# Kernel optimization log

Measured on AMD Instinct MI355X. Metric: run time of the kernel, lower is better.

The kernel has to match this reference:

```python
import jax, jax.numpy as jnp
import numpy as np

N, E, G = 50000, 200000, 1000
EPS = 1e-5
NEG_SLOPE = 0.2


def setup_inputs() -> dict:
    key = jax.random.key(0)
    ks = jax.random.split(key, 24)
    p = lambda k, shape: jax.random.normal(k, shape, jnp.float32) * 0.05
    inp = {
        "x": jax.random.normal(ks[0], (N, 64), jnp.float32),
        "edge_index": jax.random.randint(ks[1], (2, E), 0, N, jnp.int32),
        "batch": jnp.sort(jax.random.randint(ks[2], (N,), 0, G, jnp.int32)),
        "solvent_fingerprint": jax.random.uniform(ks[3], (G, 128), jnp.float32),
        # GAT layer 1: 64 -> 4 heads x 128
        "W1": p(ks[4], (64, 512)), "a1_src": p(ks[5], (4, 128)), "a1_dst": p(ks[6], (4, 128)), "b1": jnp.zeros((512,), jnp.float32),
        "bn1_g": jnp.ones((512,), jnp.float32), "bn1_b": jnp.zeros((512,), jnp.float32),
        # GAT layer 2: 512 -> 4 heads x 256
        "W2": p(ks[7], (512, 1024)), "a2_src": p(ks[8], (4, 256)), "a2_dst": p(ks[9], (4, 256)), "b2": jnp.zeros((1024,), jnp.float32),
        "bn2_g": jnp.ones((1024,), jnp.float32), "bn2_b": jnp.zeros((1024,), jnp.float32),
        # GCN: 1024 -> 256
        "Wg": p(ks[10], (1024, 256)), "bg": jnp.zeros((256,), jnp.float32),
        "bn3_g": jnp.ones((256,), jnp.float32), "bn3_b": jnp.zeros((256,), jnp.float32),
        # MLP head
        "Ws": p(ks[11], (128, 128)), "bs": jnp.zeros((128,), jnp.float32),
        "Wf1": p(ks[12], (640, 128)), "bf1": jnp.zeros((128,), jnp.float32),
        "bnf_g": jnp.ones((128,), jnp.float32), "bnf_b": jnp.zeros((128,), jnp.float32),
        "Wf2": p(ks[13], (128, 1)), "bf2": jnp.zeros((1,), jnp.float32),
    }
    return inp


def _batchnorm(x, g, b):
    mu = x.mean(0)
    var = x.var(0)
    return (x - mu) * jax.lax.rsqrt(var + EPS) * g + b


def _gat(x, src, dst, W, a_src, a_dst, b, H, C):
    n = x.shape[0]
    h = (x @ W).reshape(n, H, C)                      # [N,H,C]
    al_s = (h * a_src).sum(-1)                        # [N,H]
    al_d = (h * a_dst).sum(-1)                        # [N,H]
    e = jax.nn.leaky_relu(al_s[src] + al_d[dst], NEG_SLOPE)   # [E,H]
    m = jax.ops.segment_max(e, dst, num_segments=n)
    ex = jnp.exp(e - m[dst])
    s = jax.ops.segment_sum(ex, dst, num_segments=n)
    alpha = ex / jnp.maximum(s[dst], 1e-16)
    out = jax.ops.segment_sum(h[src] * alpha[..., None], dst, num_segments=n)  # [N,H,C]
    return out.reshape(n, H * C) + b


def _gcn(x, src, dst, W, b):
    n = x.shape[0]
    h = x @ W
    deg = jax.ops.segment_sum(jnp.ones_like(dst, jnp.float32), dst, num_segments=n)
    dinv = jax.lax.rsqrt(jnp.maximum(deg, 1.0))
    norm = dinv[src] * dinv[dst]
    return jax.ops.segment_sum(h[src] * norm[:, None], dst, num_segments=n) + b


def reference(x, edge_index, batch, solvent_fingerprint,
              W1, a1_src, a1_dst, b1, bn1_g, bn1_b,
              W2, a2_src, a2_dst, b2, bn2_g, bn2_b,
              Wg, bg, bn3_g, bn3_b,
              Ws, bs, Wf1, bf1, bnf_g, bnf_b, Wf2, bf2):
    n = x.shape[0]
    loops = jnp.arange(n, dtype=edge_index.dtype)
    src = jnp.concatenate([edge_index[0], loops])
    dst = jnp.concatenate([edge_index[1], loops])

    h = _gat(x, src, dst, W1, a1_src, a1_dst, b1, 4, 128)
    h = jax.nn.relu(_batchnorm(h, bn1_g, bn1_b))
    h = _gat(h, src, dst, W2, a2_src, a2_dst, b2, 4, 256)
    h = jax.nn.relu(_batchnorm(h, bn2_g, bn2_b))
    h = _gcn(h, src, dst, Wg, bg)
    h = jax.nn.relu(_batchnorm(h, bn3_g, bn3_b))

    cnt = jax.ops.segment_sum(jnp.ones((n,), jnp.float32), batch, num_segments=G)
    gap = jax.ops.segment_sum(h, batch, num_segments=G) / jnp.maximum(cnt, 1.0)[:, None]
    gmp = jax.ops.segment_max(h, batch, num_segments=G)
    gmp = jnp.where(jnp.isfinite(gmp), gmp, 0.0)

    solv = jax.nn.relu(solvent_fingerprint @ Ws + bs)
    z = jnp.concatenate([gap, gmp, solv], axis=1)          # [G,640]
    z = jax.nn.relu(_batchnorm(z @ Wf1 + bf1, bnf_g, bnf_b))
    # dropout: identity in eval/deterministic reference
    return jax.nn.sigmoid(z @ Wf2 + bf2)
```

## Files before the change

kernel.cpp:

```cpp
#include <hip/hip_runtime.h>
#include <cmath>

#define LEAK 0.2f
#define BN_EPS 1e-5f

static inline int cdiv(long long a, long long b){ return (int)((a + b - 1) / b); }

typedef __attribute__((ext_vector_type(8))) short bf16x8;
typedef __attribute__((ext_vector_type(4))) float f32x4;

__device__ __forceinline__ float bf2f(unsigned short u){
    return __uint_as_float(((unsigned int)u) << 16);
}
__device__ __forceinline__ unsigned short f2bf(float f){
    unsigned int u = __float_as_uint(f);
    u += 0x7FFFu + ((u >> 16) & 1u);
    return (unsigned short)(u >> 16);
}

#define GLOAD_LDS16(gsrc, ldst) \
    __builtin_amdgcn_global_load_lds( \
        (const __attribute__((address_space(1))) unsigned int*)(gsrc), \
        (__attribute__((address_space(3))) unsigned int*)(ldst), 16, 0, 0)

__global__ __launch_bounds__(256) void gemm_mfma(
    const unsigned short* __restrict__ A, const unsigned short* __restrict__ Bt,
    unsigned short* __restrict__ D, int M, int K, int lda, int ldb, int ldc,
    int NX, int NYT)
{
    const int id = blockIdx.x;
    const int xcd = id & 7;
    const int j = id >> 3;
    const int bx = j % NX;
    const int by = (j / NX) * 8 + xcd;
    if (by >= NYT) return;

    __shared__ unsigned short As[128 * 64];
    __shared__ unsigned short Bs[128 * 64];
    const int t = threadIdx.x;
    const int row0 = by * 128, col0 = bx * 128;
    const int lane = t & 63, wv = t >> 6;
    const int wm = (wv >> 1) << 6, wn = (wv & 1) << 6;
    const int lm = lane & 15, lq = lane >> 4;

    const int sr  = t >> 3;
    const int scs = (t & 7) << 3;
    const int gsw = (((t & 7) ^ (sr & 7)) << 3);
    const unsigned short* ap[4];
    const unsigned short* bp[4];
    unsigned short* la[4];
    unsigned short* lb[4];
    #pragma unroll
    for (int q = 0; q < 4; ++q) {
        int r = sr + q * 32;
        int gra = row0 + r; if (gra >= M) gra = M - 1;
        ap[q] = A  + (size_t)gra * lda + gsw;
        bp[q] = Bt + (size_t)(col0 + r) * ldb + gsw;
        la[q] = &As[r * 64 + scs];
        lb[q] = &Bs[r * 64 + scs];
    }

    f32x4 acc[4][4] = {};
    const int rx = lm & 7;

    for (int k0 = 0; k0 < K; k0 += 64) {
        #pragma unroll
        for (int q = 0; q < 4; ++q) {
            GLOAD_LDS16(ap[q] + k0, la[q]);
            GLOAD_LDS16(bp[q] + k0, lb[q]);
        }
        __syncthreads();

        #pragma unroll
        for (int kk = 0; kk < 2; ++kk) {
            const int ck = (((kk << 2) + lq) ^ rx) << 3;
            bf16x8 af[4], bfr[4];
            #pragma unroll
            for (int mi = 0; mi < 4; ++mi)
                af[mi] = *(const bf16x8*)&As[(wm + mi * 16 + lm) * 64 + ck];
            #pragma unroll
            for (int ni = 0; ni < 4; ++ni)
                bfr[ni] = *(const bf16x8*)&Bs[(wn + ni * 16 + lm) * 64 + ck];
            #pragma unroll
            for (int mi = 0; mi < 4; ++mi)
                #pragma unroll
                for (int ni = 0; ni < 4; ++ni)
                    acc[mi][ni] = __builtin_amdgcn_mfma_f32_16x16x32_bf16(
                        af[mi], bfr[ni], acc[mi][ni], 0, 0, 0);
        }
        __syncthreads();
    }

    #pragma unroll
    for (int mi = 0; mi < 4; ++mi) {
        int row_b = row0 + wm + mi * 16 + lq * 4;
        #pragma unroll
        for (int ni = 0; ni < 4; ++ni) {
            int col = col0 + wn + ni * 16 + lm;
            #pragma unroll
            for (int r = 0; r < 4; ++r) {
                int row = row_b + r;
                if (row < M) D[(size_t)row * ldc + col] = f2bf(acc[mi][ni][r]);
            }
        }
    }
}

__global__ __launch_bounds__(256) void logits_valu(
    const unsigned short* __restrict__ A, const unsigned short* __restrict__ vat,
    float* __restrict__ C, int M, int K)
{
    __shared__ unsigned short vs[8 * 512];
    const int t = threadIdx.x;
    for (int i = t; i < K; i += 256)
        *(bf16x8*)&vs[i * 8] = *(const bf16x8*)(vat + (size_t)i * 8);
    __syncthreads();

    const int lane = t & 63;
    const int w = blockIdx.x * 4 + (t >> 6);
    const int Gl = K >> 3;
    const int rpw = 64 / Gl;
    const int sub = lane / Gl;
    const int li = lane - sub * Gl;
    long long row = (long long)w * rpw + sub;
    if (row >= M) return;

    bf16x8 hv = *(const bf16x8*)(A + row * K + li * 8);
    float hf[8];
    #pragma unroll
    for (int j = 0; j < 8; ++j) hf[j] = bf2f((unsigned short)hv[j]);

    float s[8];
    #pragma unroll
    for (int o = 0; o < 8; ++o) {
        bf16x8 v = *(const bf16x8*)&vs[o * K + li * 8];
        float acc = 0.f;
        #pragma unroll
        for (int j = 0; j < 8; ++j) acc += hf[j] * bf2f((unsigned short)v[j]);
        s[o] = acc;
    }
    for (int off = Gl >> 1; off; off >>= 1) {
        #pragma unroll
        for (int o = 0; o < 8; ++o) s[o] += __shfl_xor(s[o], off);
    }
    #pragma unroll
    for (int o = 0; o < 8; ++o)
        if (li == o) C[row * 8 + o] = s[o];
}

__global__ void convT(const float* __restrict__ W, unsigned short* __restrict__ Wt, int K, int Nc)
{
    int i = blockIdx.x * blockDim.x + threadIdx.x;
    if (i >= K * Nc) return;
    int k = i / Nc, n = i - k * Nc;
    Wt[(size_t)n * K + k] = f2bf(W[i]);
}

template<bool RELU>
__global__ __launch_bounds__(256) void gemm_small(
    const float* __restrict__ A, const float* __restrict__ B,
    const float* __restrict__ bias, float* __restrict__ C,
    int M, int K, int lda, int ldb, int ldc)
{
    __shared__ float As[2][640];
    const int t = threadIdx.x;
    const int r = t >> 7, c = t & 127;
    const int row0 = blockIdx.x * 2;
    for (int i = t; i < 2 * K; i += 256) {
        int rr = i / K, kk = i - rr * K;
        int gr = row0 + rr;
        As[rr][kk] = (gr < M) ? A[(size_t)gr * lda + kk] : 0.f;
    }
    __syncthreads();
    float acc0 = 0.f, acc1 = 0.f;
    for (int k = 0; k < K; k += 8) {
        float4 a0 = *reinterpret_cast<const float4*>(&As[r][k]);
        float4 a1 = *reinterpret_cast<const float4*>(&As[r][k + 4]);
        acc0 += a0.x * B[(size_t)(k + 0) * ldb + c];
        acc1 += a0.y * B[(size_t)(k + 1) * ldb + c];
        acc0 += a0.z * B[(size_t)(k + 2) * ldb + c];
        acc1 += a0.w * B[(size_t)(k + 3) * ldb + c];
        acc0 += a1.x * B[(size_t)(k + 4) * ldb + c];
        acc1 += a1.y * B[(size_t)(k + 5) * ldb + c];
        acc0 += a1.z * B[(size_t)(k + 6) * ldb + c];
        acc1 += a1.w * B[(size_t)(k + 7) * ldb + c];
    }
    int row = row0 + r;
    if (row < M) {
        float v = acc0 + acc1;
        if (bias) v += bias[c];
        if (RELU) v = fmaxf(v, 0.f);
        C[(size_t)row * ldc + c] = v;
    }
}

__global__ void compute_va_bf(const float* __restrict__ W, const float* __restrict__ a_s,
                              const float* __restrict__ a_d, unsigned short* __restrict__ vat,
                              int K, int HC, int C)
{
    int w = (int)(((long long)blockIdx.x * blockDim.x + threadIdx.x) >> 6);
    int lane = threadIdx.x & 63;
    if (w >= K * 4) return;
    int k = w >> 2, h = w & 3;
    const float* wp = W + (size_t)k * HC + h * C;
    const float* as = a_s + h * C;
    const float* ad = a_d + h * C;
    float s = 0.f, d = 0.f;
    for (int c = lane; c < C; c += 64) {
        float v = wp[c];
        s += v * as[c];
        d += v * ad[c];
    }
    #pragma unroll
    for (int off = 32; off; off >>= 1) {
        s += __shfl_down(s, off);
        d += __shfl_down(d, off);
    }
    if (lane == 0) {
        vat[(size_t)h * K + k] = f2bf(s);
        vat[(size_t)(4 + h) * K + k] = f2bf(d);
    }
}

__device__ __forceinline__ int e_src(const int* es, int E, int k){ return k < E ? es[k] : k - E; }
__device__ __forceinline__ int e_dst(const int* ed, int E, int k){ return k < E ? ed[k] : k - E; }

__global__ void fill_i32(int* __restrict__ p, int v, int n)
{
    int i = blockIdx.x * blockDim.x + threadIdx.x;
    if (i < n) p[i] = v;
}

__global__ void hist_dst(const int* __restrict__ ed, int E, int* __restrict__ cnt)
{
    int k = blockIdx.x * blockDim.x + threadIdx.x;
    if (k < E) atomicAdd(&cnt[ed[k]], 1);
}

__global__ __launch_bounds__(256) void scan_blk(const int* __restrict__ cnt,
                                                int* __restrict__ rowptr,
                                                int* __restrict__ bsums, int n)
{
    __shared__ int ts[256];
    const int t = threadIdx.x;
    const int i0 = blockIdx.x * 1024 + t * 4;
    int4 v = {0, 0, 0, 0};
    if (i0 + 3 < n) v = *reinterpret_cast<const int4*>(cnt + i0);
    else {
        if (i0 + 0 < n) v.x = cnt[i0 + 0];
        if (i0 + 1 < n) v.y = cnt[i0 + 1];
        if (i0 + 2 < n) v.z = cnt[i0 + 2];
        if (i0 + 3 < n) v.w = cnt[i0 + 3];
    }
    int lsum = v.x + v.y + v.z + v.w;
    ts[t] = lsum;
    __syncthreads();
    #pragma unroll
    for (int off = 1; off < 256; off <<= 1) {
        int u = (t >= off) ? ts[t - off] : 0;
        __syncthreads();
        ts[t] += u;
        __syncthreads();
    }
    int excl = ts[t] - lsum;
    if (i0 + 0 < n) rowptr[i0 + 0] = excl;
    if (i0 + 1 < n) rowptr[i0 + 1] = excl + v.x;
    if (i0 + 2 < n) rowptr[i0 + 2] = excl + v.x + v.y;
    if (i0 + 3 < n) rowptr[i0 + 3] = excl + v.x + v.y + v.z;
    if (t == 255) bsums[blockIdx.x] = ts[255];
}

__global__ __launch_bounds__(256) void scan_tops(int* __restrict__ bsums,
                                                 int* __restrict__ rowptr, int nb, int n)
{
    __shared__ int ts[256];
    const int t = threadIdx.x;
    int v = (t < nb) ? bsums[t] : 0;
    ts[t] = v;
    __syncthreads();
    #pragma unroll
    for (int off = 1; off < 256; off <<= 1) {
        int u = (t >= off) ? ts[t - off] : 0;
        __syncthreads();
        ts[t] += u;
        __syncthreads();
    }
    if (t < nb) bsums[t] = ts[t] - v;
    if (t == 255) rowptr[n] = ts[255];
}

__global__ void scan_add(int* __restrict__ rowptr, int* __restrict__ cursor,
                         const int* __restrict__ bsums, int n)
{
    int i = blockIdx.x * blockDim.x + threadIdx.x;
    if (i >= n) return;
    int r = rowptr[i] + bsums[i >> 10];
    rowptr[i] = r;
    cursor[i] = r;
}

__global__ void csr_scatter(const int* __restrict__ es, const int* __restrict__ ed,
                            int E, int Etot, int* __restrict__ cursor,
                            int* __restrict__ col, int* __restrict__ dstarr)
{
    int k = blockIdx.x * blockDim.x + threadIdx.x;
    if (k >= Etot) return;
    int sn = e_src(es, E, k), dn = e_dst(ed, E, k);
    int pos = atomicAdd(&cursor[dn], 1);
    col[pos] = sn;
    dstarr[pos] = dn;
}

__global__ void dinv_from_rowptr(const int* __restrict__ rowptr, float* __restrict__ dinv, int n)
{
    int i = blockIdx.x * blockDim.x + threadIdx.x;
    if (i < n) dinv[i] = rsqrtf(fmaxf((float)(rowptr[i + 1] - rowptr[i]), 1.f));
}

__global__ void grp_lb(const int* __restrict__ batch, int N, int G_, int* __restrict__ gptr)
{
    int g = blockIdx.x * blockDim.x + threadIdx.x;
    if (g > G_) return;
    if (g == G_) { gptr[G_] = N; return; }
    int lo = 0, hi = N;
    while (lo < hi) { int mid = (lo + hi) >> 1; if (batch[mid] < g) lo = mid + 1; else hi = mid; }
    gptr[g] = lo;
}

__global__ void edge_exp4(const int* __restrict__ col, const int* __restrict__ dstarr,
                          int Etot, const float* __restrict__ alsd, float* __restrict__ exq)
{
    int p = blockIdx.x * blockDim.x + threadIdx.x;
    if (p >= Etot) return;
    int sn = col[p], dn = dstarr[p];
    #pragma unroll
    for (int h = 0; h < 4; ++h) {
        float t = alsd[sn * 8 + h] + alsd[dn * 8 + 4 + h];
        t = (t >= 0.f) ? t : LEAK * t;
        exq[(size_t)h * Etot + p] = __expf(t);
    }
}

__global__ void gat_gather_all(const int* __restrict__ rowptr, const int* __restrict__ col,
                               const unsigned short* __restrict__ h,
                               const float* __restrict__ exq, int Etot,
                               unsigned short* __restrict__ out, int N)
{
    int w = (int)(((long long)blockIdx.x * blockDim.x + threadIdx.x) >> 6);
    int lane = threadIdx.x & 63;
    if (w >= N) return;
    const float* exp_p = exq + (size_t)(lane >> 4) * Etot;
    int r0 = rowptr[w], r1 = rowptr[w + 1];
    float acc[8] = {};
    float ssum = 0.f;
    int e = r0;
    for (; e + 1 < r1; e += 2) {
        int sn0 = col[e], sn1 = col[e + 1];
        float a0 = exp_p[e], a1 = exp_p[e + 1];
        bf16x8 hv0 = *(const bf16x8*)(h + (size_t)sn0 * 512 + lane * 8);
        bf16x8 hv1 = *(const bf16x8*)(h + (size_t)sn1 * 512 + lane * 8);
        ssum += a0 + a1;
        #pragma unroll
        for (int j = 0; j < 8; ++j)
            acc[j] += bf2f((unsigned short)hv0[j]) * a0 + bf2f((unsigned short)hv1[j]) * a1;
    }
    if (e < r1) {
        int sn = col[e];
        float a = exp_p[e];
        bf16x8 hv = *(const bf16x8*)(h + (size_t)sn * 512 + lane * 8);
        ssum += a;
        #pragma unroll
        for (int j = 0; j < 8; ++j) acc[j] += bf2f((unsigned short)hv[j]) * a;
    }
    float inv = 1.f / fmaxf(ssum, 1e-16f);
    bf16x8 o;
    #pragma unroll
    for (int j = 0; j < 8; ++j) o[j] = (short)f2bf(acc[j] * inv);
    *(bf16x8*)(out + (size_t)w * 512 + lane * 8) = o;
}

__global__ void gat_gather512_bf2(const int* __restrict__ rowptr, const int* __restrict__ col,
                                  const unsigned short* __restrict__ h, int ldh,
                                  const float* __restrict__ exq0, const float* __restrict__ exq1,
                                  unsigned short* __restrict__ out, int N)
{
    int w = (int)(((long long)blockIdx.x * blockDim.x + threadIdx.x) >> 6);
    int lane = threadIdx.x & 63;
    if (w >= N) return;
    int r0 = rowptr[w], r1 = rowptr[w + 1];
    float s0 = 0.f, s1 = 0.f;
    float a00=0.f,a01=0.f,a02=0.f,a03=0.f;
    float a10=0.f,a11=0.f,a12=0.f,a13=0.f;
    int e = r0;
    for (; e + 1 < r1; e += 2) {
        int sA = col[e], sB = col[e + 1];
        float w0A = exq0[e], w0B = exq0[e + 1];
        float w1A = exq1[e], w1B = exq1[e + 1];
        const unsigned short* pA = h + (size_t)sA * ldh + lane * 4;
        const unsigned short* pB = h + (size_t)sB * ldh + lane * 4;
        ushort4 hA0 = *reinterpret_cast<const ushort4*>(pA);
        ushort4 hA1 = *reinterpret_cast<const ushort4*>(pA + 256);
        ushort4 hB0 = *reinterpret_cast<const ushort4*>(pB);
        ushort4 hB1 = *reinterpret_cast<const ushort4*>(pB + 256);
        s0 += w0A + w0B; s1 += w1A + w1B;
        a00 += bf2f(hA0.x) * w0A + bf2f(hB0.x) * w0B;
        a01 += bf2f(hA0.y) * w0A + bf2f(hB0.y) * w0B;
        a02 += bf2f(hA0.z) * w0A + bf2f(hB0.z) * w0B;
        a03 += bf2f(hA0.w) * w0A + bf2f(hB0.w) * w0B;
        a10 += bf2f(hA1.x) * w1A + bf2f(hB1.x) * w1B;
        a11 += bf2f(hA1.y) * w1A + bf2f(hB1.y) * w1B;
        a12 += bf2f(hA1.z) * w1A + bf2f(hB1.z) * w1B;
        a13 += bf2f(hA1.w) * w1A + bf2f(hB1.w) * w1B;
    }
    if (e < r1) {
        int sA = col[e];
        float w0A = exq0[e], w1A = exq1[e];
        const unsigned short* pA = h + (size_t)sA * ldh + lane * 4;
        ushort4 hA0 = *reinterpret_cast<const ushort4*>(pA);
        ushort4 hA1 = *reinterpret_cast<const ushort4*>(pA + 256);
        s0 += w0A; s1 += w1A;
        a00 += bf2f(hA0.x) * w0A; a01 += bf2f(hA0.y) * w0A;
        a02 += bf2f(hA0.z) * w0A; a03 += bf2f(hA0.w) * w0A;
        a10 += bf2f(hA1.x) * w1A; a11 += bf2f(hA1.y) * w1A;
        a12 += bf2f(hA1.z) * w1A; a13 += bf2f(hA1.w) * w1A;
    }
    float i0 = 1.f / fmaxf(s0, 1e-16f);
    float i1 = 1.f / fmaxf(s1, 1e-16f);
    ushort4 o0, o1;
    o0.x = f2bf(a00 * i0); o0.y = f2bf(a01 * i0);
    o0.z = f2bf(a02 * i0); o0.w = f2bf(a03 * i0);
    o1.x = f2bf(a10 * i1); o1.y = f2bf(a11 * i1);
    o1.z = f2bf(a12 * i1); o1.w = f2bf(a13 * i1);
    unsigned short* op = out + (size_t)w * 512 + lane * 4;
    *reinterpret_cast<ushort4*>(op)       = o0;
    *reinterpret_cast<ushort4*>(op + 256) = o1;
}

__global__ void gcn_gather256(const int* __restrict__ rowptr, const int* __restrict__ col,
                              const unsigned short* __restrict__ h,
                              const float* __restrict__ dinv,
                              unsigned short* __restrict__ out, int N)
{
    int w = (int)(((long long)blockIdx.x * blockDim.x + threadIdx.x) >> 6);
    int lane = threadIdx.x & 63;
    if (w >= N) return;
    int r0 = rowptr[w], r1 = rowptr[w + 1];
    float a0 = 0.f, a1 = 0.f, a2 = 0.f, a3 = 0.f;
    int e = r0;
    for (; e + 1 < r1; e += 2) {
        int sn0 = col[e], sn1 = col[e + 1];
        float w0 = dinv[sn0], w1 = dinv[sn1];
        ushort4 hv0 = *reinterpret_cast<const ushort4*>(h + (size_t)sn0 * 256 + lane * 4);
        ushort4 hv1 = *reinterpret_cast<const ushort4*>(h + (size_t)sn1 * 256 + lane * 4);
        a0 += bf2f(hv0.x) * w0 + bf2f(hv1.x) * w1;
        a1 += bf2f(hv0.y) * w0 + bf2f(hv1.y) * w1;
        a2 += bf2f(hv0.z) * w0 + bf2f(hv1.z) * w1;
        a3 += bf2f(hv0.w) * w0 + bf2f(hv1.w) * w1;
    }
    if (e < r1) {
        int sn = col[e];
        float wv = dinv[sn];
        ushort4 hv = *reinterpret_cast<const ushort4*>(h + (size_t)sn * 256 + lane * 4);
        a0 += bf2f(hv.x) * wv; a1 += bf2f(hv.y) * wv;
        a2 += bf2f(hv.z) * wv; a3 += bf2f(hv.w) * wv;
    }
    float dn = dinv[w];
    ushort4 o;
    o.x = f2bf(a0 * dn); o.y = f2bf(a1 * dn);
    o.z = f2bf(a2 * dn); o.w = f2bf(a3 * dn);
    *reinterpret_cast<ushort4*>(out + (size_t)w * 256 + lane * 4) = o;
}

template<int D>
__global__ __launch_bounds__(256) void bn_part(
    const float* __restrict__ x, float* __restrict__ ps, float* __restrict__ pq,
    int M, int Y)
{
    constexpr int DG = D / 4;
    constexpr int P  = 256 / DG;
    const int t = threadIdx.x;
    const int cg = t % DG, ph = t / DG;
    const int y = blockIdx.y;
    const int rows_per = (M + Y - 1) / Y;
    const int r0 = y * rows_per;
    const int r1 = min(r0 + rows_per, M);
    float s0=0,s1=0,s2=0,s3=0,q0=0,q1=0,q2=0,q3=0;
    for (int r = r0 + ph; r < r1; r += P) {
        float4 v = *reinterpret_cast<const float4*>(x + (size_t)r * D + cg * 4);
        s0+=v.x; s1+=v.y; s2+=v.z; s3+=v.w;
        q0+=v.x*v.x; q1+=v.y*v.y; q2+=v.z*v.z; q3+=v.w*v.w;
    }
    __shared__ float ls[P][D];
    __shared__ float lq[P][D];
    ls[ph][cg*4+0]=s0; ls[ph][cg*4+1]=s1; ls[ph][cg*4+2]=s2; ls[ph][cg*4+3]=s3;
    lq[ph][cg*4+0]=q0; lq[ph][cg*4+1]=q1; lq[ph][cg*4+2]=q2; lq[ph][cg*4+3]=q3;
    __syncthreads();
    if (ph == 0) {
        #pragma unroll
        for (int j = 0; j < 4; ++j) {
            float ss = 0.f, qq = 0.f;
            #pragma unroll
            for (int p = 0; p < P; ++p) { ss += ls[p][cg*4+j]; qq += lq[p][cg*4+j]; }
            ps[(size_t)y * D + cg*4 + j] = ss;
            pq[(size_t)y * D + cg*4 + j] = qq;
        }
    }
}

template<int D>
__global__ __launch_bounds__(256) void bn_part_bf(
    const unsigned short* __restrict__ x, int ldx,
    float* __restrict__ ps, float* __restrict__ pq, int M, int Y)
{
    constexpr int DG = D / 4;
    constexpr int P  = 256 / DG;
    const int t = threadIdx.x;
    const int cg = t % DG, ph = t / DG;
    const int y = blockIdx.y;
    const int rows_per = (M + Y - 1) / Y;
    const int r0 = y * rows_per;
    const int r1 = min(r0 + rows_per, M);
    float s0=0,s1=0,s2=0,s3=0,q0=0,q1=0,q2=0,q3=0;
    for (int r = r0 + ph; r < r1; r += P) {
        ushort4 u = *reinterpret_cast<const ushort4*>(x + (size_t)r * ldx + cg * 4);
        float vx = bf2f(u.x), vy = bf2f(u.y), vz = bf2f(u.z), vw = bf2f(u.w);
        s0+=vx; s1+=vy; s2+=vz; s3+=vw;
        q0+=vx*vx; q1+=vy*vy; q2+=vz*vz; q3+=vw*vw;
    }
    __shared__ float ls[P][D];
    __shared__ float lq[P][D];
    ls[ph][cg*4+0]=s0; ls[ph][cg*4+1]=s1; ls[ph][cg*4+2]=s2; ls[ph][cg*4+3]=s3;
    lq[ph][cg*4+0]=q0; lq[ph][cg*4+1]=q1; lq[ph][cg*4+2]=q2; lq[ph][cg*4+3]=q3;
    __syncthreads();
    if (ph == 0) {
        #pragma unroll
        for (int j = 0; j < 4; ++j) {
            float ss = 0.f, qq = 0.f;
            #pragma unroll
            for (int p = 0; p < P; ++p) { ss += ls[p][cg*4+j]; qq += lq[p][cg*4+j]; }
            ps[(size_t)y * D + cg*4 + j] = ss;
            pq[(size_t)y * D + cg*4 + j] = qq;
        }
    }
}

template<int D>
__global__ __launch_bounds__(256) void bn_reduce_fin(
    const float* __restrict__ ps, const float* __restrict__ pq,
    const float* __restrict__ g, const float* __restrict__ b,
    float* __restrict__ scale, float* __restrict__ shift, int Y, float invM)
{
    const int t = threadIdx.x;
    const int cl = t & 63;
    const int c = blockIdx.x * 64 + cl;
    const int ph = t >> 6;
    float s = 0.f, q = 0.f;
    for (int y = ph; y < Y; y += 4) {
        s += ps[(size_t)y * D + c];
        q += pq[(size_t)y * D + c];
    }
    __shared__ float ls[4][64];
    __shared__ float lq[4][64];
    ls[ph][cl] = s; lq[ph][cl] = q;
    __syncthreads();
    if (ph == 0) {
        s = ls[0][cl] + ls[1][cl] + ls[2][cl] + ls[3][cl];
        q = lq[0][cl] + lq[1][cl] + lq[2][cl] + lq[3][cl];
        float mu = s * invM;
        float var = q * invM - mu * mu;
        float rs = rsqrtf(var + BN_EPS) * g[c];
        scale[c] = rs;
        shift[c] = b[c] - mu * rs;
    }
}

__global__ void bn_apply_bfbf(const unsigned short* __restrict__ x,
                              const float* __restrict__ scale, const float* __restrict__ shift,
                              unsigned short* __restrict__ dst, int total4, int Cb4,
                              int ldx, int ldd)
{
    int i = blockIdx.x * blockDim.x + threadIdx.x;
    if (i >= total4) return;
    int r = i / Cb4, c4 = (i - r * Cb4) * 4;
    ushort4 u = *reinterpret_cast<const ushort4*>(x + (size_t)r * ldx + c4);
    float4 sc = *reinterpret_cast<const float4*>(scale + c4);
    float4 sh = *reinterpret_cast<const float4*>(shift + c4);
    ushort4 o;
    o.x = f2bf(fmaxf(bf2f(u.x) * sc.x + sh.x, 0.f));
    o.y = f2bf(fmaxf(bf2f(u.y) * sc.y + sh.y, 0.f));
    o.z = f2bf(fmaxf(bf2f(u.z) * sc.z + sh.z, 0.f));
    o.w = f2bf(fmaxf(bf2f(u.w) * sc.w + sh.w, 0.f));
    *reinterpret_cast<ushort4*>(dst + (size_t)r * ldd + c4) = o;
}

__global__ void conv_f2b4(const float* __restrict__ src, unsigned short* __restrict__ dst, int n4)
{
    int i = blockIdx.x * blockDim.x + threadIdx.x;
    if (i >= n4) return;
    float4 v = *reinterpret_cast<const float4*>(src + (size_t)i * 4);
    ushort4 o = { f2bf(v.x), f2bf(v.y), f2bf(v.z), f2bf(v.w) };
    *reinterpret_cast<ushort4*>(dst + (size_t)i * 4) = o;
}

__global__ __launch_bounds__(256) void pool_gather_bn(const unsigned short* __restrict__ h,
                                                      const float* __restrict__ scale,
                                                      const float* __restrict__ shift,
                                                      const int* __restrict__ gptr,
                                                      float* __restrict__ z, int G_)
{
    int g = blockIdx.x;
    int c = threadIdx.x;
    int r0 = gptr[g], r1 = gptr[g + 1];
    float sc = scale[c], sh = shift[c];
    float s = 0.f, m = 0.f;
    int i = r0;
    for (; i + 1 < r1; i += 2) {
        float v0 = fmaxf(bf2f(h[(size_t)i * 256 + c]) * sc + sh, 0.f);
        float v1 = fmaxf(bf2f(h[(size_t)(i + 1) * 256 + c]) * sc + sh, 0.f);
        s += v0 + v1;
        m = fmaxf(m, fmaxf(v0, v1));
    }
    if (i < r1) {
        float v = fmaxf(bf2f(h[(size_t)i * 256 + c]) * sc + sh, 0.f);
        s += v;
        m = fmaxf(m, v);
    }
    float cnt = fmaxf((float)(r1 - r0), 1.f);
    z[(size_t)g * 640 + c] = s / cnt;
    z[(size_t)g * 640 + 256 + c] = m;
}

__global__ void final_head_bn(const float* __restrict__ f1,
                              const float* __restrict__ scale, const float* __restrict__ shift,
                              const float* __restrict__ Wf2, const float* __restrict__ bf2,
                              float* __restrict__ out, int G_)
{
    int w = (int)(((long long)blockIdx.x * blockDim.x + threadIdx.x) >> 6);
    int lane = threadIdx.x & 63;
    if (w >= G_) return;
    float s = 0.f;
    #pragma unroll
    for (int q = 0; q < 2; ++q) {
        int c = lane + q * 64;
        float v = fmaxf(f1[(size_t)w * 128 + c] * scale[c] + shift[c], 0.f);
        s += v * Wf2[c];
    }
    #pragma unroll
    for (int off = 32; off; off >>= 1) s += __shfl_down(s, off);
    if (lane == 0) out[w] = 1.f / (1.f + __expf(-(s + bf2[0])));
}

__global__ void sentinel(float* __restrict__ out, int n, float v)
{
    int i = blockIdx.x * blockDim.x + threadIdx.x;
    if (i < n) out[i] = v;
}

extern "C" void kernel_launch(void* const* d_in, const int* in_sizes, int n_in,
                              void* d_out, int out_size, void* d_ws, size_t ws_size,
                              hipStream_t stream)
{
    const float* x    = (const float*)d_in[0];
    const int*   ei   = (const int*)d_in[1];
    const int*   batch= (const int*)d_in[2];
    const float* sfp  = (const float*)d_in[3];
    const float* W1   = (const float*)d_in[4];
    const float* a1s  = (const float*)d_in[5];
    const float* a1d  = (const float*)d_in[6];
    const float* bn1g = (const float*)d_in[8];
    const float* bn1b = (const float*)d_in[9];
    const float* W2   = (const float*)d_in[10];
    const float* a2s  = (const float*)d_in[11];
    const float* a2d  = (const float*)d_in[12];
    const float* bn2g = (const float*)d_in[14];
    const float* bn2b = (const float*)d_in[15];
    const float* Wg   = (const float*)d_in[16];
    const float* bn3g = (const float*)d_in[18];
    const float* bn3b = (const float*)d_in[19];
    const float* Wsm  = (const float*)d_in[20];
    const float* bsm  = (const float*)d_in[21];
    const float* Wf1  = (const float*)d_in[22];
    const float* bnfg = (const float*)d_in[24];
    const float* bnfb = (const float*)d_in[25];
    const float* Wf2  = (const float*)d_in[26];
    const float* bf2  = (const float*)d_in[27];
    float* outp = (float*)d_out;

    const int N    = in_sizes[0] / 64;
    const int E    = in_sizes[1] / 2;
    const int G_   = in_sizes[3] / 128;
    const int Etot = E + N;
    const int* esrc = ei;
    const int* edst = ei + E;
    const int YB = 256;
    const int NB = cdiv(N, 1024);
    const int NYT = cdiv(N, 128);
    const int NYT8 = cdiv(NYT, 8) * 8;

    float* ws = (float*)d_ws;
    size_t off = 0;
    float* accA  = ws + off; off += (size_t)N * 256;
    float* h3acc = ws + off; off += (size_t)N * 256;
    unsigned short* g1b   = (unsigned short*)accA;
    unsigned short* g3b   = (unsigned short*)accA;
    unsigned short* h2all = (unsigned short*)accA;
    unsigned short* R1 = (unsigned short*)(ws + off); off += (size_t)N * 256;
    unsigned short* h1b = R1;
    unsigned short* o1n = R1;
    unsigned short* hb  = (unsigned short*)(ws + off); off += (size_t)N * 128;
    unsigned short* xb  = (unsigned short*)(ws + off); off += (size_t)N * 32;
    float* alsd = ws + off; off += (size_t)N * 8;
    float* dinv = ws + off; off += N;
    float* bsc = ws + off; off += 1024;
    float* bsh = ws + off; off += 1024;
    float* ps  = ws + off; off += (size_t)YB * 512;
    float* pq  = ws + off; off += (size_t)YB * 512;
    float* z   = ws + off; off += (size_t)G_ * 640;
    float* f1  = ws + off; off += (size_t)G_ * 128;
    int* rowptr = (int*)(ws + off); off += (size_t)(N + 1);
    int* colc   = (int*)(ws + off); off += (size_t)Etot;
    int* dstarr = (int*)(ws + off); off += (size_t)Etot;
    float* exq  = ws + off; off += (size_t)Etot * 4;
    int* gptr   = (int*)(ws + off); off += (size_t)(G_ + 1);
    int* bsums  = (int*)(ws + off); off += 256;
    off = (off + 3) & ~(size_t)3;
    unsigned short* vat1 = (unsigned short*)(ws + off); off += 128 * 64 / 2;
    unsigned short* vat2 = (unsigned short*)(ws + off); off += 128 * 512 / 2;
    unsigned short* W1t = (unsigned short*)(ws + off); off += 64 * 512 / 2;
    unsigned short* W2t = (unsigned short*)(ws + off); off += 512 * 1024 / 2;
    unsigned short* Wgt = (unsigned short*)(ws + off); off += 1024 * 256 / 2;
    int* cursor = (int*)alsd;
    size_t need = off * 4;
    if (ws_size < need) {
        sentinel<<<cdiv(out_size, 256), 256, 0, stream>>>(outp, out_size, (float)(ws_size >> 20));
        return;
    }

    const int BLK = 256;
    dim3 blk(BLK);

    convT<<<cdiv(64 * 512, BLK), blk, 0, stream>>>(W1, W1t, 64, 512);
    convT<<<cdiv(512 * 1024, BLK), blk, 0, stream>>>(W2, W2t, 512, 1024);
    convT<<<cdiv(1024 * 256, BLK), blk, 0, stream>>>(Wg, Wgt, 1024, 256);
    conv_f2b4<<<cdiv((long long)N * 16, BLK), blk, 0, stream>>>(x, xb, N * 16);
    compute_va_bf<<<cdiv(64 * 4 * 64, BLK), blk, 0, stream>>>(W1, a1s, a1d, vat1, 64, 512, 128);
    compute_va_bf<<<cdiv(512 * 4 * 64, BLK), blk, 0, stream>>>(W2, a2s, a2d, vat2, 512, 1024, 256);

    fill_i32<<<cdiv(N, BLK), blk, 0, stream>>>(cursor, 1, N);
    hist_dst<<<cdiv(E, BLK), blk, 0, stream>>>(edst, E, cursor);
    scan_blk<<<NB, blk, 0, stream>>>(cursor, rowptr, bsums, N);
    scan_tops<<<1, blk, 0, stream>>>(bsums, rowptr, NB, N);
    scan_add<<<cdiv(N, BLK), blk, 0, stream>>>(rowptr, cursor, bsums, N);
    csr_scatter<<<cdiv(Etot, BLK), blk, 0, stream>>>(esrc, edst, E, Etot, cursor, colc, dstarr);
    dinv_from_rowptr<<<cdiv(N, BLK), blk, 0, stream>>>(rowptr, dinv, N);
    grp_lb<<<cdiv(G_ + 1, BLK), blk, 0, stream>>>(batch, N, G_, gptr);

    gemm_mfma<<<NYT8 * 4, blk, 0, stream>>>(xb, W1t, h1b, N, 64, 64, 64, 512, 4, NYT);
    logits_valu<<<cdiv(cdiv((long long)N * 64, 512), 4), blk, 0, stream>>>(xb, vat1, alsd, N, 64);
    edge_exp4<<<cdiv(Etot, BLK), blk, 0, stream>>>(colc, dstarr, Etot, alsd, exq);
    gat_gather_all<<<cdiv((long long)N * 64, BLK), blk, 0, stream>>>(
        rowptr, colc, h1b, exq, Etot, g1b, N);
    { dim3 g(1, YB); bn_part_bf<512><<<g, blk, 0, stream>>>(g1b, 512, ps, pq, N, YB); }
    bn_reduce_fin<512><<<8, blk, 0, stream>>>(ps, pq, bn1g, bn1b, bsc, bsh, YB, 1.f / N);
    bn_apply_bfbf<<<cdiv((long long)N * 128, BLK), blk, 0, stream>>>(
        g1b, bsc, bsh, o1n, N * 128, 128, 512, 512);

    logits_valu<<<cdiv(N, 4), blk, 0, stream>>>(o1n, vat2, alsd, N, 512);
    edge_exp4<<<cdiv(Etot, BLK), blk, 0, stream>>>(colc, dstarr, Etot, alsd, exq);

    gemm_mfma<<<NYT8 * 8, blk, 0, stream>>>(o1n, W2t, h2all, N, 512, 512, 512, 1024, 8, NYT);
    for (int pr = 0; pr < 2; ++pr) {
        gat_gather512_bf2<<<cdiv((long long)N * 64, BLK), blk, 0, stream>>>(
            rowptr, colc, h2all + pr * 512, 1024,
            exq + (size_t)(2 * pr) * Etot, exq + (size_t)(2 * pr + 1) * Etot, R1, N);
        { dim3 g(1, YB); bn_part_bf<512><<<g, blk, 0, stream>>>(R1, 512, ps, pq, N, YB); }
        bn_reduce_fin<512><<<8, blk, 0, stream>>>(ps, pq, bn2g + pr * 512, bn2b + pr * 512,
                                                  bsc + pr * 512, bsh + pr * 512, YB, 1.f / N);
        bn_apply_bfbf<<<cdiv((long long)N * 128, BLK), blk, 0, stream>>>(
            R1, bsc + pr * 512, bsh + pr * 512, h2all + pr * 512, N * 128, 128, 512, 1024);
    }
    gemm_mfma<<<NYT8 * 2, blk, 0, stream>>>(h2all, Wgt, hb, N, 1024, 1024, 1024, 256, 2, NYT);

    gcn_gather256<<<cdiv((long long)N * 64, BLK), blk, 0, stream>>>(
        rowptr, colc, hb, dinv, g3b, N);
    { dim3 g(1, YB); bn_part_bf<256><<<g, blk, 0, stream>>>(g3b, 256, ps, pq, N, YB); }
    bn_reduce_fin<256><<<4, blk, 0, stream>>>(ps, pq, bn3g, bn3b, bsc, bsh, YB, 1.f / N);

    pool_gather_bn<<<G_, blk, 0, stream>>>(g3b, bsc, bsh, gptr, z, G_);

    gemm_small<true><<<cdiv(G_, 2), blk, 0, stream>>>(
        sfp, Wsm, bsm, z + 512, G_, 128, 128, 128, 640);

    gemm_small<false><<<cdiv(G_, 2), blk, 0, stream>>>(
        z, Wf1, nullptr, f1, G_, 640, 640, 128, 128);
    { dim3 g(1, YB); bn_part<128><<<g, blk, 0, stream>>>(f1, ps, pq, G_, YB); }
    bn_reduce_fin<128><<<2, blk, 0, stream>>>(ps, pq, bnfg, bnfb, bsc, bsh, YB, 1.f / G_);
    final_head_bn<<<cdiv((long long)G_ * 64, BLK), blk, 0, stream>>>(
        f1, bsc, bsh, Wf2, bf2, outp, G_);
}
```

Before: 842.0 us.

## Aggregate raw 64-dim features per head before GAT1 projection

Reorders GAT layer 1 so attention-weighted aggregation runs over the 64-wide input features for each of the 4 heads, producing a 256-wide per-node buffer. A block-diagonal weight (512x256) then projects the aggregated features into the 512-wide output with one MFMA GEMM. Each edge now gathers 64 bf16 values instead of 512, cutting irregular gather traffic. In exchange the GEMM has K=256 instead of 64, three quarters of it multiplying zeros, and the logits launch grid is changed.

```diff
diff --git a/kernel.cpp b/kernel.cpp
--- a/kernel.cpp
+++ b/kernel.cpp
@@ -156,6 +156,16 @@
     Wt[(size_t)n * K + k] = f2bf(W[i]);
 }
 
+__global__ void conv_w1bd(const float* __restrict__ W, unsigned short* __restrict__ Wt)
+{
+    int i = blockIdx.x * blockDim.x + threadIdx.x;
+    if (i >= 512 * 256) return;
+    int o = i >> 8, k = i & 255;
+    unsigned short v = 0;
+    if ((k >> 6) == (o >> 7)) v = f2bf(W[(size_t)(k & 63) * 512 + o]);
+    Wt[i] = v;
+}
+
 template<bool RELU>
 __global__ __launch_bounds__(256) void gemm_small(
     const float* __restrict__ A, const float* __restrict__ B,
@@ -341,42 +351,49 @@
     }
 }
 
-__global__ void gat_gather_all(const int* __restrict__ rowptr, const int* __restrict__ col,
-                               const unsigned short* __restrict__ h,
-                               const float* __restrict__ exq, int Etot,
-                               unsigned short* __restrict__ out, int N)
+__global__ void gat_agg4_64(const int* __restrict__ rowptr, const int* __restrict__ col,
+                            const unsigned short* __restrict__ xb,
+                            const float* __restrict__ exq, int Etot,
+                            unsigned short* __restrict__ agg, int N)
 {
     int w = (int)(((long long)blockIdx.x * blockDim.x + threadIdx.x) >> 6);
     int lane = threadIdx.x & 63;
     if (w >= N) return;
-    const float* exp_p = exq + (size_t)(lane >> 4) * Etot;
+    const float* ex0 = exq;
+    const float* ex1 = exq + (size_t)Etot;
+    const float* ex2 = exq + (size_t)2 * Etot;
+    const float* ex3 = exq + (size_t)3 * Etot;
     int r0 = rowptr[w], r1 = rowptr[w + 1];
-    float acc[8] = {};
-    float ssum = 0.f;
+    float a0 = 0.f, a1 = 0.f, a2 = 0.f, a3 = 0.f;
+    float s0 = 0.f, s1 = 0.f, s2 = 0.f, s3 = 0.f;
     int e = r0;
     for (; e + 1 < r1; e += 2) {
-        int sn0 = col[e], sn1 = col[e + 1];
-        float a0 = exp_p[e], a1 = exp_p[e + 1];
-        bf16x8 hv0 = *(const bf16x8*)(h + (size_t)sn0 * 512 + lane * 8);
-        bf16x8 hv1 = *(const bf16x8*)(h + (size_t)sn1 * 512 + lane * 8);
-        ssum += a0 + a1;
-        #pragma unroll
-        for (int j = 0; j < 8; ++j)
-            acc[j] += bf2f((unsigned short)hv0[j]) * a0 + bf2f((unsigned short)hv1[j]) * a1;
+        int snA = col[e], snB = col[e + 1];
+        float xA = bf2f(xb[(size_t)snA * 64 + lane]);
+        float xB = bf2f(xb[(size_t)snB * 64 + lane]);
+        float w0A = ex0[e], w0B = ex0[e + 1];
+        float w1A = ex1[e], w1B = ex1[e + 1];
+        float w2A = ex2[e], w2B = ex2[e + 1];
+        float w3A = ex3[e], w3B = ex3[e + 1];
+        a0 += w0A * xA + w0B * xB;  s0 += w0A + w0B;
+        a1 += w1A * xA + w1B * xB;  s1 += w1A + w1B;
+        a2 += w2A * xA + w2B * xB;  s2 += w2A + w2B;
+        a3 += w3A * xA + w3B * xB;  s3 += w3A + w3B;
     }
     if (e < r1) {
         int sn = col[e];
-        float a = exp_p[e];
-        bf16x8 hv = *(const bf16x8*)(h + (size_t)sn * 512 + lane * 8);
-        ssum += a;
-        #pragma unroll
-        for (int j = 0; j < 8; ++j) acc[j] += bf2f((unsigned short)hv[j]) * a;
-    }
-    float inv = 1.f / fmaxf(ssum, 1e-16f);
-    bf16x8 o;
-    #pragma unroll
-    for (int j = 0; j < 8; ++j) o[j] = (short)f2bf(acc[j] * inv);
-    *(bf16x8*)(out + (size_t)w * 512 + lane * 8) = o;
+        float xA = bf2f(xb[(size_t)sn * 64 + lane]);
+        float w0 = ex0[e], w1 = ex1[e], w2 = ex2[e], w3 = ex3[e];
+        a0 += w0 * xA; s0 += w0;
+        a1 += w1 * xA; s1 += w1;
+        a2 += w2 * xA; s2 += w2;
+        a3 += w3 * xA; s3 += w3;
+    }
+    unsigned short* op = agg + (size_t)w * 256 + lane;
+    op[0]   = f2bf(a0 / fmaxf(s0, 1e-16f));
+    op[64]  = f2bf(a1 / fmaxf(s1, 1e-16f));
+    op[128] = f2bf(a2 / fmaxf(s2, 1e-16f));
+    op[192] = f2bf(a3 / fmaxf(s3, 1e-16f));
 }
 
 __global__ void gat_gather512_bf2(const int* __restrict__ rowptr, const int* __restrict__ col,
@@ -705,7 +722,6 @@
     unsigned short* g3b   = (unsigned short*)accA;
     unsigned short* h2all = (unsigned short*)accA;
     unsigned short* R1 = (unsigned short*)(ws + off); off += (size_t)N * 256;
-    unsigned short* h1b = R1;
     unsigned short* o1n = R1;
     unsigned short* hb  = (unsigned short*)(ws + off); off += (size_t)N * 128;
     unsigned short* xb  = (unsigned short*)(ws + off); off += (size_t)N * 32;
@@ -726,7 +742,7 @@
     off = (off + 3) & ~(size_t)3;
     unsigned short* vat1 = (unsigned short*)(ws + off); off += 128 * 64 / 2;
     unsigned short* vat2 = (unsigned short*)(ws + off); off += 128 * 512 / 2;
-    unsigned short* W1t = (unsigned short*)(ws + off); off += 64 * 512 / 2;
+    unsigned short* W1bdt = (unsigned short*)(ws + off); off += 512 * 256 / 2;
     unsigned short* W2t = (unsigned short*)(ws + off); off += 512 * 1024 / 2;
     unsigned short* Wgt = (unsigned short*)(ws + off); off += 1024 * 256 / 2;
     int* cursor = (int*)alsd;
@@ -739,7 +755,7 @@
     const int BLK = 256;
     dim3 blk(BLK);
 
-    convT<<<cdiv(64 * 512, BLK), blk, 0, stream>>>(W1, W1t, 64, 512);
+    conv_w1bd<<<cdiv(512 * 256, BLK), blk, 0, stream>>>(W1, W1bdt);
     convT<<<cdiv(512 * 1024, BLK), blk, 0, stream>>>(W2, W2t, 512, 1024);
     convT<<<cdiv(1024 * 256, BLK), blk, 0, stream>>>(Wg, Wgt, 1024, 256);
     conv_f2b4<<<cdiv((long long)N * 16, BLK), blk, 0, stream>>>(x, xb, N * 16);
@@ -755,11 +771,11 @@
     dinv_from_rowptr<<<cdiv(N, BLK), blk, 0, stream>>>(rowptr, dinv, N);
     grp_lb<<<cdiv(G_ + 1, BLK), blk, 0, stream>>>(batch, N, G_, gptr);
 
-    gemm_mfma<<<NYT8 * 4, blk, 0, stream>>>(xb, W1t, h1b, N, 64, 64, 64, 512, 4, NYT);
-    logits_valu<<<cdiv(cdiv((long long)N * 64, 512), 4), blk, 0, stream>>>(xb, vat1, alsd, N, 64);
+    logits_valu<<<cdiv(N, 32), blk, 0, stream>>>(xb, vat1, alsd, N, 64);
     edge_exp4<<<cdiv(Etot, BLK), blk, 0, stream>>>(colc, dstarr, Etot, alsd, exq);
-    gat_gather_all<<<cdiv((long long)N * 64, BLK), blk, 0, stream>>>(
-        rowptr, colc, h1b, exq, Etot, g1b, N);
+    gat_agg4_64<<<cdiv((long long)N * 64, BLK), blk, 0, stream>>>(
+        rowptr, colc, xb, exq, Etot, hb, N);
+    gemm_mfma<<<NYT8 * 4, blk, 0, stream>>>(hb, W1bdt, g1b, N, 256, 256, 256, 512, 4, NYT);
     { dim3 g(1, YB); bn_part_bf<512><<<g, blk, 0, stream>>>(g1b, 512, ps, pq, N, YB); }
     bn_reduce_fin<512><<<8, blk, 0, stream>>>(ps, pq, bn1g, bn1b, bsc, bsh, YB, 1.f / N);
     bn_apply_bfbf<<<cdiv((long long)N * 128, BLK), blk, 0, stream>>>(
```

Measured after the change: 840.0 us. No clear change (-0.2%).
